# Kernel tuning notes

Hardware: AMD Instinct MI355X
Metric: run time of the kernel (lower is better)

The kernel has to match this reference:

```python
import jax, jax.numpy as jnp
import numpy as np
from jax import lax

B, L, D = 2, 1024, 1024
EXPAND, N, K = 2, 16, 4          # expand, d_state, d_conv
DI = EXPAND * D                  # d_inner = 2048
R = (D + 15) // 16               # dt_rank = 64
EPS = 1e-5


def setup_inputs() -> dict:
    key = jax.random.key(0)
    ks = jax.random.split(key, 8)
    x = jax.random.normal(ks[0], (B, L, D), dtype=jnp.float32)
    ln_w = jnp.ones((D,), jnp.float32)
    ln_b = jnp.zeros((D,), jnp.float32)
    W_in = jax.random.normal(ks[1], (D, 2 * DI), jnp.float32) * (1.0 / np.sqrt(D))
    conv_w = jax.random.normal(ks[2], (DI, K), jnp.float32) * 0.2
    conv_b = jnp.zeros((DI,), jnp.float32)
    W_x = jax.random.normal(ks[3], (DI, R + 2 * N), jnp.float32) * (1.0 / np.sqrt(DI))
    W_dt = jax.random.normal(ks[4], (R, DI), jnp.float32) * (1.0 / np.sqrt(R))
    b_dt = jnp.full((DI,), -4.0, jnp.float32)  # softplus(-4) ~ 0.018 dt init
    A_log = jnp.log(jnp.broadcast_to(jnp.arange(1, N + 1, dtype=jnp.float32), (DI, N)))
    D_param = jnp.ones((DI,), jnp.float32)
    W_out = jax.random.normal(ks[5], (DI, D), jnp.float32) * (1.0 / np.sqrt(DI))
    return {"x": x, "ln_w": ln_w, "ln_b": ln_b, "W_in": W_in, "conv_w": conv_w,
            "conv_b": conv_b, "W_x": W_x, "W_dt": W_dt, "b_dt": b_dt,
            "A_log": A_log, "D_param": D_param, "W_out": W_out}


def _mamba_block(x, ln_w, ln_b, W_in, conv_w, conv_b, W_x, W_dt, b_dt, A_log, D_param, W_out):
    # pre-LayerNorm
    mu = jnp.mean(x, axis=-1, keepdims=True)
    xc = x - mu
    var = jnp.mean(xc * xc, axis=-1, keepdims=True)
    h = xc * lax.rsqrt(var + EPS) * ln_w + ln_b          # [B,L,D]

    xz = h @ W_in                                        # [B,L,2*DI]
    xi, z = xz[..., :DI], xz[..., DI:]

    # depthwise causal conv1d, kernel K, left pad K-1
    xp = jnp.pad(xi, ((0, 0), (K - 1, 0), (0, 0)))
    conv = conv_b
    for k in range(K):
        conv = conv + xp[:, k:k + L, :] * conv_w[:, k]
    u = jax.nn.silu(conv)                                # [B,L,DI]

    proj = u @ W_x                                       # [B,L,R+2N]
    dt_r = proj[..., :R]
    Bm = proj[..., R:R + N]                              # [B,L,N]
    Cm = proj[..., R + N:]                               # [B,L,N]
    dt = jax.nn.softplus(dt_r @ W_dt + b_dt)             # [B,L,DI]

    A = -jnp.exp(A_log)                                  # [DI,N]
    dA = jnp.exp(dt[..., None] * A)                      # [B,L,DI,N]
    dBu = (dt * u)[..., None] * Bm[:, :, None, :]        # [B,L,DI,N]

    def comb(e1, e2):
        a1, b1 = e1
        a2, b2 = e2
        return a1 * a2, a2 * b1 + b2

    _, hs = lax.associative_scan(comb, (dA, dBu), axis=1)  # [B,L,DI,N]
    y = jnp.einsum('bldn,bln->bld', hs, Cm) + u * D_param
    y = y * jax.nn.silu(z)
    return x + y @ W_out


def reference(x, ln_w, ln_b, W_in, conv_w, conv_b, W_x, W_dt, b_dt, A_log, D_param, W_out):
    return _mamba_block(x, ln_w, ln_b, W_in, conv_w, conv_b, W_x, W_dt, b_dt,
                        A_log, D_param, W_out)
```

## Files before the change

### kernel.cpp

```cpp
#include <hip/hip_runtime.h>
#include <hip/hip_bf16.h>
#include <math.h>

#define B_ 2
#define L_ 1024
#define D_ 1024
#define DI_ 2048
#define K_ 4
#define N_ 16
#define R_ 64
#define BL_ (B_ * L_)
#define EPS_ 1e-5f

#define IDX4(l) ((l) + (((l) >> 6) << 2))

typedef __attribute__((ext_vector_type(8))) short short8;
typedef __attribute__((ext_vector_type(4))) float f32x4;

__device__ inline unsigned short f2bf(float f) {
    unsigned u = __float_as_uint(f);
    unsigned r = (u + 0x7fffu + ((u >> 16) & 1u)) >> 16;
    return (unsigned short)r;
}
__device__ inline float bf2f(unsigned short s) {
    return __uint_as_float(((unsigned)s) << 16);
}
__device__ inline float fast_silu(float z) {
    return z * __builtin_amdgcn_rcpf(1.f + __expf(-z));
}
__device__ inline void gl_lds16(const void* g, void* l) {
    __builtin_amdgcn_global_load_lds(
        (const __attribute__((address_space(1))) void*)g,
        (__attribute__((address_space(3))) void*)l, 16, 0, 0);
}

template <int CTRL>
__device__ inline float dpp_shr(float x) {
    return __int_as_float(__builtin_amdgcn_update_dpp(
        0, __float_as_int(x), CTRL, 0xf, 0xf, true));
}
__device__ inline float row16_sum(float p) {
    p += dpp_shr<0x111>(p);
    p += dpp_shr<0x112>(p);
    p += dpp_shr<0x114>(p);
    p += dpp_shr<0x118>(p);
    return p;
}

__global__ void ln_kernel(const float* __restrict__ x, const float* __restrict__ w,
                          const float* __restrict__ b, unsigned short* __restrict__ hb) {
    int row = blockIdx.x;
    const float* xr = x + (size_t)row * D_;
    float4 v = ((const float4*)xr)[threadIdx.x];

    __shared__ float red[4];
    float s = v.x + v.y + v.z + v.w;
    for (int off = 1; off < 64; off <<= 1) s += __shfl_xor(s, off, 64);
    if ((threadIdx.x & 63) == 0) red[threadIdx.x >> 6] = s;
    __syncthreads();
    float mu = (red[0] + red[1] + red[2] + red[3]) * (1.0f / D_);
    __syncthreads();
    float cx = v.x - mu, cy = v.y - mu, cz = v.z - mu, cw = v.w - mu;
    float sq = cx*cx + cy*cy + cz*cz + cw*cw;
    for (int off = 1; off < 64; off <<= 1) sq += __shfl_xor(sq, off, 64);
    if ((threadIdx.x & 63) == 0) red[threadIdx.x >> 6] = sq;
    __syncthreads();
    float var = (red[0] + red[1] + red[2] + red[3]) * (1.0f / D_);
    float rstd = rsqrtf(var + EPS_);

    float4 wv = ((const float4*)w)[threadIdx.x];
    float4 bv = ((const float4*)b)[threadIdx.x];
    ushort4 o;
    o.x = f2bf(cx * rstd * wv.x + bv.x);
    o.y = f2bf(cy * rstd * wv.y + bv.y);
    o.z = f2bf(cz * rstd * wv.z + bv.z);
    o.w = f2bf(cw * rstd * wv.w + bv.w);
    ((ushort4*)(hb + (size_t)row * D_))[threadIdx.x] = o;
}

__global__ void transpose_cast(const float* __restrict__ W, unsigned short* __restrict__ WT,
                               int K, int N) {
    __shared__ float tile[32][33];
    int k0 = blockIdx.y * 32, n0 = blockIdx.x * 32;
    int tr = threadIdx.x >> 5;
    int tc = threadIdx.x & 31;
#pragma unroll
    for (int i = 0; i < 4; ++i)
        tile[tr + i*8][tc] = W[(size_t)(k0 + tr + i*8) * N + n0 + tc];
    __syncthreads();
#pragma unroll
    for (int i = 0; i < 4; ++i)
        WT[(size_t)(n0 + tr + i*8) * K + k0 + tc] = f2bf(tile[tc][tr + i*8]);
}

template <int BN, int MODE>
__global__ __launch_bounds__(256) void mfma_gemm_bt(
        const unsigned short* __restrict__ A,  int lda,
        const unsigned short* __restrict__ BT, int ldb,
        float* __restrict__ C, int ldc, int Kchunk) {
    constexpr int NT = BN / 32;
    __shared__ unsigned short As[128 * 32];
    __shared__ unsigned short Bs[BN * 32];

    int tid = threadIdx.x;
    int wave = tid >> 6, lane = tid & 63;
    int lane15 = lane & 15, quad = lane >> 4;
    int wr = wave >> 1, wc = wave & 1;

    int m0 = blockIdx.y * 128;
    int n0 = blockIdx.x * BN;
    int kbeg = blockIdx.z * Kchunk;
    int kend = kbeg + Kchunk;

    f32x4 acc[4][NT];
#pragma unroll
    for (int i = 0; i < 4; ++i)
#pragma unroll
        for (int j = 0; j < NT; ++j) acc[i][j] = (f32x4){0.f, 0.f, 0.f, 0.f};

    constexpr int ACALLS = 8;
    constexpr int BCALLS = BN * 4 / 64;

    for (int k0 = kbeg; k0 < kend; k0 += 32) {
        __syncthreads();
        for (int c = wave; c < ACALLS + BCALLS; c += 4) {
            if (c < ACALLS) {
                int cell = c * 64 + lane;
                int m = cell >> 2, s = cell & 3;
                int q = s ^ (m & 3) ^ ((m >> 2) & 3);
                gl_lds16(A + (size_t)(m0 + m) * lda + k0 + q * 8, &As[c * 512]);
            } else {
                int cell = (c - ACALLS) * 64 + lane;
                int n = cell >> 2, s = cell & 3;
                int q = s ^ (n & 3) ^ ((n >> 2) & 3);
                gl_lds16(BT + (size_t)(n0 + n) * ldb + k0 + q * 8, &Bs[(c - ACALLS) * 512]);
            }
        }
        __syncthreads();

        short8 af[4], bfr[NT];
#pragma unroll
        for (int i = 0; i < 4; ++i) {
            int m = wr * 64 + i * 16 + lane15;
            int s = quad ^ (m & 3) ^ ((m >> 2) & 3);
            af[i] = *(const short8*)&As[m * 32 + s * 8];
        }
#pragma unroll
        for (int j = 0; j < NT; ++j) {
            int n = wc * (NT * 16) + j * 16 + lane15;
            int s = quad ^ (n & 3) ^ ((n >> 2) & 3);
            bfr[j] = *(const short8*)&Bs[n * 32 + s * 8];
        }
#pragma unroll
        for (int i = 0; i < 4; ++i)
#pragma unroll
            for (int j = 0; j < NT; ++j)
                acc[i][j] = __builtin_amdgcn_mfma_f32_16x16x32_bf16(af[i], bfr[j], acc[i][j], 0, 0, 0);
    }

#pragma unroll
    for (int i = 0; i < 4; ++i) {
        int row = m0 + wr * 64 + i * 16 + quad * 4;
#pragma unroll
        for (int j = 0; j < NT; ++j) {
            int col = n0 + wc * (NT * 16) + j * 16 + lane15;
#pragma unroll
            for (int r = 0; r < 4; ++r) {
                float v = acc[i][j][r];
                size_t off = (size_t)(row + r) * ldc + col;
                if (MODE == 0) C[off] = v;
                else atomicAdd(&C[off], v);
            }
        }
    }
}

template <int EPI>
__global__ __launch_bounds__(256) void gemm_kernel(
        const float* __restrict__ A, int lda,
        const float* __restrict__ Bm, int ldb,
        float* __restrict__ C, int ldc,
        int M, int Nn, int Kk,
        const float* __restrict__ bias) {
    const int BK = 16;
    __shared__ float As[BK][64 + 4];
    __shared__ float Bs[BK][64];

    int tid = threadIdx.x;
    int m0 = blockIdx.y * 64;
    int n0 = blockIdx.x * 64;
    int ar = tid >> 2, ak = (tid & 3) << 2;
    int kb = tid >> 4, bc = (tid & 15) << 2;
    int ty = tid >> 4, tx = tid & 15;

    float acc[4][4] = {};
    for (int k0 = 0; k0 < Kk; k0 += BK) {
        const float* Ap = A + (size_t)(m0 + ar) * lda + (k0 + ak);
        float4 av = *(const float4*)Ap;
        As[ak + 0][ar] = av.x; As[ak + 1][ar] = av.y;
        As[ak + 2][ar] = av.z; As[ak + 3][ar] = av.w;

        const float* Bp = Bm + (size_t)(k0 + kb) * ldb + n0 + bc;
        float4 bv = *(const float4*)Bp;
        Bs[kb][bc + 0] = bv.x; Bs[kb][bc + 1] = bv.y;
        Bs[kb][bc + 2] = bv.z; Bs[kb][bc + 3] = bv.w;
        __syncthreads();
#pragma unroll
        for (int kk = 0; kk < BK; ++kk) {
            float a[4], bb[4];
#pragma unroll
            for (int i = 0; i < 4; ++i) a[i] = As[kk][ty * 4 + i];
#pragma unroll
            for (int j = 0; j < 4; ++j) bb[j] = Bs[kk][tx * 4 + j];
#pragma unroll
            for (int i = 0; i < 4; ++i)
#pragma unroll
                for (int j = 0; j < 4; ++j)
                    acc[i][j] = fmaf(a[i], bb[j], acc[i][j]);
        }
        __syncthreads();
    }
#pragma unroll
    for (int i = 0; i < 4; ++i) {
        int row = m0 + ty * 4 + i;
#pragma unroll
        for (int j = 0; j < 4; ++j) {
            int col = n0 + tx * 4 + j;
            float v = acc[i][j];
            if (EPI == 1) {
                v += bias[col];
                v = fmaxf(v, 0.f) + __logf(1.f + __expf(-fabsf(v)));
            }
            C[(size_t)row * ldc + col] = v;
        }
    }
}

__global__ void conv_silu_kernel(const float* __restrict__ xz, const float* __restrict__ cw,
                                 const float* __restrict__ cb, unsigned short* __restrict__ ub) {
    int idx = blockIdx.x * blockDim.x + threadIdx.x;
    int c = idx & (DI_ - 1);
    int bl = idx >> 11;
    int l = bl & (L_ - 1);
    float4 w4 = ((const float4*)cw)[c];
    float acc = cb[c];
    const float* base = xz + (size_t)bl * (2 * DI_) + c;
    if (l >= 3) {
        acc = fmaf(base[-(size_t)3 * 2 * DI_], w4.x, acc);
        acc = fmaf(base[-(size_t)2 * 2 * DI_], w4.y, acc);
        acc = fmaf(base[-(size_t)1 * 2 * DI_], w4.z, acc);
        acc = fmaf(base[0],                    w4.w, acc);
    } else {
        if (l >= 2) acc = fmaf(*(base - 2 * 2 * DI_), w4.y, acc);
        if (l >= 1) acc = fmaf(*(base - 1 * 2 * DI_), w4.z, acc);
        acc = fmaf(base[0], w4.w, acc);
    }
    ub[idx] = f2bf(fast_silu(acc));
}

__global__ void prep_v3(const float* __restrict__ dt, const unsigned short* __restrict__ ub,
                        const float* __restrict__ xz, const float* __restrict__ Dp,
                        float2* __restrict__ dtduT, unsigned int* __restrict__ szdT) {
    __shared__ float t_dt[32][33];
    __shared__ float t_du[32][33];
    __shared__ unsigned int t_sd[32][33];
    int bl0 = blockIdx.y * 32, c0 = blockIdx.x * 32;
    int r = threadIdx.x >> 5;
    int col = threadIdx.x & 31;
    float dpv = Dp[c0 + col];
#pragma unroll
    for (int i = 0; i < 4; ++i) {
        int bl = bl0 + r + i*8;
        float d = dt[(size_t)bl * DI_ + c0 + col];
        float uu = bf2f(ub[(size_t)bl * DI_ + c0 + col]);
        float z = xz[(size_t)bl * (2 * DI_) + DI_ + c0 + col];
        float sz = fast_silu(z);
        t_dt[r + i*8][col] = d;
        t_du[r + i*8][col] = d * uu;
        t_sd[r + i*8][col] = ((unsigned)f2bf(uu * dpv * sz) << 16) | (unsigned)f2bf(sz);
    }
    __syncthreads();
#pragma unroll
    for (int i = 0; i < 4; ++i) {
        int c = c0 + r + i*8;
        dtduT[(size_t)c * BL_ + bl0 + col] = make_float2(t_dt[col][r + i*8], t_du[col][r + i*8]);
        szdT [(size_t)c * BL_ + bl0 + col] = t_sd[col][r + i*8];
    }
}

__global__ void bct2_kernel(const float* __restrict__ proj, float2* __restrict__ bcti) {
    int t = threadIdx.x;
    int bl = blockIdx.x * 16 + (t >> 4);
    int n = t & 15;
    float Bv = proj[(size_t)bl * 96 + R_ + n];
    float Cv = proj[(size_t)bl * 96 + R_ + N_ + n];
    bcti[(size_t)bl * 16 + n] = make_float2(Bv, Cv);
}

__global__ __launch_bounds__(256) void scan_v4(
        const float2* __restrict__ dtduT, const unsigned int* __restrict__ szdT,
        const float2* __restrict__ bcti, const float* __restrict__ A_log,
        unsigned short* __restrict__ yzT) {
    int bc = blockIdx.x;
    int b = bc >> 11;
    int c = bc & (DI_ - 1);
    int t = threadIdx.x;
    int chunk = t >> 4;
    int n = t & 15;

    __shared__ float dd[(L_ + 32) * 2];
    __shared__ float sA[16][16];
    __shared__ float sB[16][16];
    __shared__ float ps[L_ + 64];

    const size_t tb = (size_t)c * BL_ + (size_t)b * L_;

    {
        int l = t * 4;
        const float4* g = (const float4*)(dtduT + tb + l);
        float4 a0 = g[0], a1 = g[1];
        int il2 = l + ((l >> 6) << 1);
        *(float4*)&dd[il2 * 2]     = a0;
        *(float4*)&dd[il2 * 2 + 4] = a1;
    }
    __syncthreads();

    float A = -__expf(A_log[c * N_ + n]);
    int l0 = chunk * 64;
    const float* ddp = &dd[(l0 + 2 * chunk) * 2];
    const float* bcf = (const float*)(bcti + ((size_t)b * L_ + l0) * 16 + n);

    float a = 1.f, acc = 0.f;
#pragma unroll
    for (int q = 0; q < 16; ++q) {
        float4 d0 = *(const float4*)(ddp + q * 8);
        float4 d1 = *(const float4*)(ddp + q * 8 + 4);
        float b0 = bcf[(q*4 + 0) * 32];
        float b1 = bcf[(q*4 + 1) * 32];
        float b2 = bcf[(q*4 + 2) * 32];
        float b3 = bcf[(q*4 + 3) * 32];
        float e;
        e = __expf(d0.x * A); a *= e; acc = fmaf(e, acc, d0.y * b0);
        e = __expf(d0.z * A); a *= e; acc = fmaf(e, acc, d0.w * b1);
        e = __expf(d1.x * A); a *= e; acc = fmaf(e, acc, d1.y * b2);
        e = __expf(d1.z * A); a *= e; acc = fmaf(e, acc, d1.w * b3);
    }
    sA[chunk][n] = a;
    sB[chunk][n] = acc;
    __syncthreads();

    if (t < 16) {
        float hc = 0.f;
#pragma unroll
        for (int j = 0; j < 16; ++j) {
            float aj = sA[j][t];
            float bj = sB[j][t];
            sB[j][t] = hc;
            hc = fmaf(aj, hc, bj);
        }
    }
    __syncthreads();
    float h = sB[chunk][n];

    float* psb = &ps[IDX4(l0)];
    const float2* bcp = bcti + ((size_t)b * L_ + l0) * 16 + n;
#pragma unroll
    for (int q = 0; q < 16; ++q) {
        float4 d0 = *(const float4*)(ddp + q * 8);
        float4 d1 = *(const float4*)(ddp + q * 8 + 4);
        float2 bc0 = bcp[(q*4 + 0) * 16];
        float2 bc1 = bcp[(q*4 + 1) * 16];
        float2 bc2 = bcp[(q*4 + 2) * 16];
        float2 bc3 = bcp[(q*4 + 3) * 16];
        float e, p0, p1, p2, p3;
        e = __expf(d0.x * A); h = fmaf(e, h, d0.y * bc0.x); p0 = row16_sum(h * bc0.y);
        e = __expf(d0.z * A); h = fmaf(e, h, d0.w * bc1.x); p1 = row16_sum(h * bc1.y);
        e = __expf(d1.x * A); h = fmaf(e, h, d1.y * bc2.x); p2 = row16_sum(h * bc2.y);
        e = __expf(d1.z * A); h = fmaf(e, h, d1.w * bc3.x); p3 = row16_sum(h * bc3.y);
        if (n == 15) *(float4*)&psb[q * 4] = (float4){p0, p1, p2, p3};
    }
    __syncthreads();

    {
        int l = t * 4;
        int il = IDX4(l);
        float4 p4 = *(const float4*)&ps[il];
        uint4 sd4 = *(const uint4*)(szdT + tb + l);
        ushort4 o;
        o.x = f2bf(p4.x * bf2f((unsigned short)(sd4.x & 0xffff)) + bf2f((unsigned short)(sd4.x >> 16)));
        o.y = f2bf(p4.y * bf2f((unsigned short)(sd4.y & 0xffff)) + bf2f((unsigned short)(sd4.y >> 16)));
        o.z = f2bf(p4.z * bf2f((unsigned short)(sd4.z & 0xffff)) + bf2f((unsigned short)(sd4.z >> 16)));
        o.w = f2bf(p4.w * bf2f((unsigned short)(sd4.w & 0xffff)) + bf2f((unsigned short)(sd4.w >> 16)));
        *(ushort4*)(yzT + tb + l) = o;
    }
}

__global__ void transpose_y(const unsigned short* __restrict__ yzT, unsigned short* __restrict__ yz) {
    __shared__ unsigned short t[32][33];
    int c0 = blockIdx.y * 32, bl0 = blockIdx.x * 32;
    int r = threadIdx.x >> 5;
    int col = threadIdx.x & 31;
#pragma unroll
    for (int i = 0; i < 4; ++i)
        t[r + i*8][col] = yzT[(size_t)(c0 + r + i*8) * BL_ + bl0 + col];
    __syncthreads();
#pragma unroll
    for (int i = 0; i < 4; ++i)
        yz[(size_t)(bl0 + r + i*8) * DI_ + c0 + col] = t[col][r + i*8];
}

extern "C" void kernel_launch(void* const* d_in, const int* in_sizes, int n_in,
                              void* d_out, int out_size, void* d_ws, size_t ws_size,
                              hipStream_t stream) {
    const float* x       = (const float*)d_in[0];
    const float* ln_w    = (const float*)d_in[1];
    const float* ln_b    = (const float*)d_in[2];
    const float* W_in    = (const float*)d_in[3];
    const float* conv_w  = (const float*)d_in[4];
    const float* conv_b  = (const float*)d_in[5];
    const float* W_x     = (const float*)d_in[6];
    const float* W_dt    = (const float*)d_in[7];
    const float* b_dt    = (const float*)d_in[8];
    const float* A_log   = (const float*)d_in[9];
    const float* D_param = (const float*)d_in[10];
    const float* W_out   = (const float*)d_in[11];
    float* out = (float*)d_out;

    uint8_t* p = (uint8_t*)d_ws;
    unsigned short* hb    = (unsigned short*)p;  p += (size_t)BL_ * D_ * 2;
    unsigned short* WinT  = (unsigned short*)p;  p += (size_t)4096 * 1024 * 2;
    float*          xz    = (float*)p;           p += (size_t)BL_ * 2 * DI_ * 4;
    unsigned short* ub    = (unsigned short*)p;  p += (size_t)BL_ * DI_ * 2;
    unsigned short* WxT   = (unsigned short*)p;  p += (size_t)96 * DI_ * 2;
    float*          proj  = (float*)p;           p += (size_t)BL_ * 96 * 4;
    float*          dt    = (float*)p;           p += (size_t)BL_ * DI_ * 4;
    unsigned short* WoutT = (unsigned short*)p;  p += (size_t)1024 * DI_ * 2;
    float2*         dtduT = (float2*)p;          p += (size_t)BL_ * DI_ * 8;
    unsigned int*   szdT  = (unsigned int*)p;    p += (size_t)BL_ * DI_ * 4;
    float2*         bcti  = (float2*)p;          p += (size_t)BL_ * 16 * 8;
    unsigned short* yzT   = (unsigned short*)p;  p += (size_t)BL_ * DI_ * 2;
    unsigned short* yzb   = (unsigned short*)d_ws;

    hipMemsetAsync(proj, 0, (size_t)BL_ * 96 * 4, stream);
    hipMemcpyAsync(out, x, (size_t)BL_ * D_ * 4, hipMemcpyDeviceToDevice, stream);

    transpose_cast<<<dim3(4096 / 32, 1024 / 32), 256, 0, stream>>>(W_in, WinT, 1024, 4096);
    transpose_cast<<<dim3(96 / 32, DI_ / 32), 256, 0, stream>>>(W_x, WxT, DI_, 96);
    transpose_cast<<<dim3(1024 / 32, DI_ / 32), 256, 0, stream>>>(W_out, WoutT, DI_, 1024);

    ln_kernel<<<BL_, 256, 0, stream>>>(x, ln_w, ln_b, hb);

    mfma_gemm_bt<128, 0><<<dim3(4096 / 128, BL_ / 128, 1), 256, 0, stream>>>(
        hb, 1024, WinT, 1024, xz, 4096, 1024);

    conv_silu_kernel<<<(BL_ * DI_) / 256, 256, 0, stream>>>(xz, conv_w, conv_b, ub);

    mfma_gemm_bt<96, 1><<<dim3(1, BL_ / 128, 16), 256, 0, stream>>>(
        ub, DI_, WxT, DI_, proj, 96, 128);

    gemm_kernel<1><<<dim3(DI_ / 64, BL_ / 64), 256, 0, stream>>>(
        proj, 96, W_dt, DI_, dt, DI_, BL_, DI_, R_, b_dt);

    prep_v3<<<dim3(DI_ / 32, BL_ / 32), 256, 0, stream>>>(dt, ub, xz, D_param, dtduT, szdT);
    bct2_kernel<<<BL_ / 16, 256, 0, stream>>>(proj, bcti);

    scan_v4<<<B_ * DI_, 256, 0, stream>>>(dtduT, szdT, bcti, A_log, yzT);

    transpose_y<<<dim3(BL_ / 32, DI_ / 32), 256, 0, stream>>>(yzT, yzb);

    mfma_gemm_bt<128, 1><<<dim3(1024 / 128, BL_ / 128, 2), 256, 0, stream>>>(
        yzb, DI_, WoutT, DI_, out, 1024, 1024);
}
```

Measured before the change: 323.6 us.

## Fuse dt GEMM with scan prep, split in-proj epilogue, merge weight casts

The in-projection GEMM epilogue now writes xi in fp32 and silu(z) in bf16 to separate buffers, so later kernels no longer re-read the full fp32 z half. The dt projection GEMM is fused with softplus and the transposed dt/du/skip packing, which removes the fp32 dt round trip and the separate prep kernel. The scan now handles two channels per block and reads B/C straight from proj, so the bct2 kernel goes away. The three weight transposes are merged into one launch. Risks include register and LDS pressure in the fused kernels and strided uncoalesced B/C reads from proj inside the scan.

Result: faster. 286.7 us (-11.4%).

```diff
diff --git a/kernel.cpp b/kernel.cpp
--- a/kernel.cpp
+++ b/kernel.cpp
@@ -78,10 +78,17 @@
     ((ushort4*)(hb + (size_t)row * D_))[threadIdx.x] = o;
 }
 
-__global__ void transpose_cast(const float* __restrict__ W, unsigned short* __restrict__ WT,
-                               int K, int N) {
+__global__ void transpose_cast_all(const float* __restrict__ W_in, const float* __restrict__ W_x,
+                                   const float* __restrict__ W_out,
+                                   unsigned short* __restrict__ WinT, unsigned short* __restrict__ WxT,
+                                   unsigned short* __restrict__ WoutT) {
+    int bid = blockIdx.x;
+    const float* W; unsigned short* WT; int K, N, bx, by;
+    if (bid < 4096)      { W = W_in;  WT = WinT;  K = 1024; N = 4096; bx = bid & 127; by = bid >> 7; }
+    else if (bid < 4288) { int id = bid - 4096; W = W_x;  WT = WxT;  K = DI_; N = 96;   bx = id % 3;  by = id / 3; }
+    else                 { int id = bid - 4288; W = W_out; WT = WoutT; K = DI_; N = 1024; bx = id & 31; by = id >> 5; }
     __shared__ float tile[32][33];
-    int k0 = blockIdx.y * 32, n0 = blockIdx.x * 32;
+    int k0 = by * 32, n0 = bx * 32;
     int tr = threadIdx.x >> 5;
     int tc = threadIdx.x & 31;
 #pragma unroll
@@ -97,7 +104,8 @@
 __global__ __launch_bounds__(256) void mfma_gemm_bt(
         const unsigned short* __restrict__ A,  int lda,
         const unsigned short* __restrict__ BT, int ldb,
-        float* __restrict__ C, int ldc, int Kchunk) {
+        float* __restrict__ C, int ldc, int Kchunk,
+        float* __restrict__ xi, unsigned short* __restrict__ sz) {
     constexpr int NT = BN / 32;
     __shared__ unsigned short As[128 * 32];
     __shared__ unsigned short Bs[BN * 32];
@@ -167,76 +175,21 @@
 #pragma unroll
             for (int r = 0; r < 4; ++r) {
                 float v = acc[i][j][r];
-                size_t off = (size_t)(row + r) * ldc + col;
-                if (MODE == 0) C[off] = v;
-                else atomicAdd(&C[off], v);
+                int rr = row + r;
+                if (MODE == 0) {
+                    C[(size_t)rr * ldc + col] = v;
+                } else if (MODE == 1) {
+                    atomicAdd(&C[(size_t)rr * ldc + col], v);
+                } else {
+                    if (col < DI_) xi[(size_t)rr * DI_ + col] = v;
+                    else           sz[(size_t)rr * DI_ + (col - DI_)] = f2bf(fast_silu(v));
+                }
             }
         }
     }
 }
 
-template <int EPI>
-__global__ __launch_bounds__(256) void gemm_kernel(
-        const float* __restrict__ A, int lda,
-        const float* __restrict__ Bm, int ldb,
-        float* __restrict__ C, int ldc,
-        int M, int Nn, int Kk,
-        const float* __restrict__ bias) {
-    const int BK = 16;
-    __shared__ float As[BK][64 + 4];
-    __shared__ float Bs[BK][64];
-
-    int tid = threadIdx.x;
-    int m0 = blockIdx.y * 64;
-    int n0 = blockIdx.x * 64;
-    int ar = tid >> 2, ak = (tid & 3) << 2;
-    int kb = tid >> 4, bc = (tid & 15) << 2;
-    int ty = tid >> 4, tx = tid & 15;
-
-    float acc[4][4] = {};
-    for (int k0 = 0; k0 < Kk; k0 += BK) {
-        const float* Ap = A + (size_t)(m0 + ar) * lda + (k0 + ak);
-        float4 av = *(const float4*)Ap;
-        As[ak + 0][ar] = av.x; As[ak + 1][ar] = av.y;
-        As[ak + 2][ar] = av.z; As[ak + 3][ar] = av.w;
-
-        const float* Bp = Bm + (size_t)(k0 + kb) * ldb + n0 + bc;
-        float4 bv = *(const float4*)Bp;
-        Bs[kb][bc + 0] = bv.x; Bs[kb][bc + 1] = bv.y;
-        Bs[kb][bc + 2] = bv.z; Bs[kb][bc + 3] = bv.w;
-        __syncthreads();
-#pragma unroll
-        for (int kk = 0; kk < BK; ++kk) {
-            float a[4], bb[4];
-#pragma unroll
-            for (int i = 0; i < 4; ++i) a[i] = As[kk][ty * 4 + i];
-#pragma unroll
-            for (int j = 0; j < 4; ++j) bb[j] = Bs[kk][tx * 4 + j];
-#pragma unroll
-            for (int i = 0; i < 4; ++i)
-#pragma unroll
-                for (int j = 0; j < 4; ++j)
-                    acc[i][j] = fmaf(a[i], bb[j], acc[i][j]);
-        }
-        __syncthreads();
-    }
-#pragma unroll
-    for (int i = 0; i < 4; ++i) {
-        int row = m0 + ty * 4 + i;
-#pragma unroll
-        for (int j = 0; j < 4; ++j) {
-            int col = n0 + tx * 4 + j;
-            float v = acc[i][j];
-            if (EPI == 1) {
-                v += bias[col];
-                v = fmaxf(v, 0.f) + __logf(1.f + __expf(-fabsf(v)));
-            }
-            C[(size_t)row * ldc + col] = v;
-        }
-    }
-}
-
-__global__ void conv_silu_kernel(const float* __restrict__ xz, const float* __restrict__ cw,
+__global__ void conv_silu_kernel(const float* __restrict__ xi, const float* __restrict__ cw,
                                  const float* __restrict__ cb, unsigned short* __restrict__ ub) {
     int idx = blockIdx.x * blockDim.x + threadIdx.x;
     int c = idx & (DI_ - 1);
@@ -244,115 +197,189 @@
     int l = bl & (L_ - 1);
     float4 w4 = ((const float4*)cw)[c];
     float acc = cb[c];
-    const float* base = xz + (size_t)bl * (2 * DI_) + c;
+    const float* base = xi + (size_t)bl * DI_ + c;
     if (l >= 3) {
-        acc = fmaf(base[-(size_t)3 * 2 * DI_], w4.x, acc);
-        acc = fmaf(base[-(size_t)2 * 2 * DI_], w4.y, acc);
-        acc = fmaf(base[-(size_t)1 * 2 * DI_], w4.z, acc);
-        acc = fmaf(base[0],                    w4.w, acc);
+        acc = fmaf(base[-(size_t)3 * DI_], w4.x, acc);
+        acc = fmaf(base[-(size_t)2 * DI_], w4.y, acc);
+        acc = fmaf(base[-(size_t)1 * DI_], w4.z, acc);
+        acc = fmaf(base[0],                w4.w, acc);
     } else {
-        if (l >= 2) acc = fmaf(*(base - 2 * 2 * DI_), w4.y, acc);
-        if (l >= 1) acc = fmaf(*(base - 1 * 2 * DI_), w4.z, acc);
+        if (l >= 2) acc = fmaf(*(base - 2 * DI_), w4.y, acc);
+        if (l >= 1) acc = fmaf(*(base - 1 * DI_), w4.z, acc);
         acc = fmaf(base[0], w4.w, acc);
     }
     ub[idx] = f2bf(fast_silu(acc));
 }
 
-__global__ void prep_v3(const float* __restrict__ dt, const unsigned short* __restrict__ ub,
-                        const float* __restrict__ xz, const float* __restrict__ Dp,
-                        float2* __restrict__ dtduT, unsigned int* __restrict__ szdT) {
-    __shared__ float t_dt[32][33];
-    __shared__ float t_du[32][33];
-    __shared__ unsigned int t_sd[32][33];
-    int bl0 = blockIdx.y * 32, c0 = blockIdx.x * 32;
-    int r = threadIdx.x >> 5;
-    int col = threadIdx.x & 31;
-    float dpv = Dp[c0 + col];
+__global__ __launch_bounds__(256) void dtprep(
+        const float* __restrict__ proj, const float* __restrict__ W_dt,
+        const float* __restrict__ b_dt, const unsigned short* __restrict__ ub,
+        const unsigned short* __restrict__ szb, const float* __restrict__ Dp,
+        float2* __restrict__ dtduT, unsigned int* __restrict__ szdT) {
+    __shared__ alignas(16) unsigned char smem[64 * 65 * 8];
+    float (*As)[68] = reinterpret_cast<float(*)[68]>(smem);
+    float (*Bs)[64] = reinterpret_cast<float(*)[64]>(smem + 4352);
+    float2 (*T2)[65] = reinterpret_cast<float2(*)[65]>(smem);
+    unsigned int (*TU)[65] = reinterpret_cast<unsigned int(*)[65]>(smem);
+
+    int tid = threadIdx.x;
+    int n0 = blockIdx.x * 64;
+    int m0 = blockIdx.y * 64;
+    int ar = tid >> 2, ak = (tid & 3) << 2;
+    int kb = tid >> 4, bc = (tid & 15) << 2;
+    int ty = tid >> 4, tx = tid & 15;
+
+    float acc[4][4] = {};
+#pragma unroll
+    for (int k0 = 0; k0 < R_; k0 += 16) {
+        float4 av = *(const float4*)&proj[(size_t)(m0 + ar) * 96 + k0 + ak];
+        As[ak + 0][ar] = av.x; As[ak + 1][ar] = av.y;
+        As[ak + 2][ar] = av.z; As[ak + 3][ar] = av.w;
+        float4 bv = *(const float4*)&W_dt[(size_t)(k0 + kb) * DI_ + n0 + bc];
+        Bs[kb][bc + 0] = bv.x; Bs[kb][bc + 1] = bv.y;
+        Bs[kb][bc + 2] = bv.z; Bs[kb][bc + 3] = bv.w;
+        __syncthreads();
+#pragma unroll
+        for (int kk = 0; kk < 16; ++kk) {
+            float a[4], bb[4];
+#pragma unroll
+            for (int i = 0; i < 4; ++i) a[i] = As[kk][ty * 4 + i];
+#pragma unroll
+            for (int j = 0; j < 4; ++j) bb[j] = Bs[kk][tx * 4 + j];
+#pragma unroll
+            for (int i = 0; i < 4; ++i)
+#pragma unroll
+                for (int j = 0; j < 4; ++j)
+                    acc[i][j] = fmaf(a[i], bb[j], acc[i][j]);
+        }
+        __syncthreads();
+    }
+
+    float4 bd = *(const float4*)&b_dt[n0 + tx * 4];
+    float4 dp4 = *(const float4*)&Dp[n0 + tx * 4];
+    float bda[4] = {bd.x, bd.y, bd.z, bd.w};
+    float dpa[4] = {dp4.x, dp4.y, dp4.z, dp4.w};
+    float2 d2[4][4];
+    unsigned int su[4][4];
 #pragma unroll
     for (int i = 0; i < 4; ++i) {
-        int bl = bl0 + r + i*8;
-        float d = dt[(size_t)bl * DI_ + c0 + col];
-        float uu = bf2f(ub[(size_t)bl * DI_ + c0 + col]);
-        float z = xz[(size_t)bl * (2 * DI_) + DI_ + c0 + col];
-        float sz = fast_silu(z);
-        t_dt[r + i*8][col] = d;
-        t_du[r + i*8][col] = d * uu;
-        t_sd[r + i*8][col] = ((unsigned)f2bf(uu * dpv * sz) << 16) | (unsigned)f2bf(sz);
-    }
-    __syncthreads();
-#pragma unroll
-    for (int i = 0; i < 4; ++i) {
-        int c = c0 + r + i*8;
-        dtduT[(size_t)c * BL_ + bl0 + col] = make_float2(t_dt[col][r + i*8], t_du[col][r + i*8]);
-        szdT [(size_t)c * BL_ + bl0 + col] = t_sd[col][r + i*8];
-    }
-}
-
-__global__ void bct2_kernel(const float* __restrict__ proj, float2* __restrict__ bcti) {
-    int t = threadIdx.x;
-    int bl = blockIdx.x * 16 + (t >> 4);
-    int n = t & 15;
-    float Bv = proj[(size_t)bl * 96 + R_ + n];
-    float Cv = proj[(size_t)bl * 96 + R_ + N_ + n];
-    bcti[(size_t)bl * 16 + n] = make_float2(Bv, Cv);
-}
-
-__global__ __launch_bounds__(256) void scan_v4(
+        int bl = m0 + ty * 4 + i;
+        ushort4 u4 = *(const ushort4*)&ub[(size_t)bl * DI_ + n0 + tx * 4];
+        ushort4 s4 = *(const ushort4*)&szb[(size_t)bl * DI_ + n0 + tx * 4];
+        unsigned short ua[4] = {u4.x, u4.y, u4.z, u4.w};
+        unsigned short sa[4] = {s4.x, s4.y, s4.z, s4.w};
+#pragma unroll
+        for (int j = 0; j < 4; ++j) {
+            float v = acc[i][j] + bda[j];
+            float dtv = fmaxf(v, 0.f) + __logf(1.f + __expf(-fabsf(v)));
+            float uu = bf2f(ua[j]);
+            float szv = bf2f(sa[j]);
+            d2[i][j] = make_float2(dtv, dtv * uu);
+            su[i][j] = ((unsigned)f2bf(uu * dpa[j] * szv) << 16) | (unsigned)f2bf(szv);
+        }
+    }
+
+#pragma unroll
+    for (int i = 0; i < 4; ++i)
+#pragma unroll
+        for (int j = 0; j < 4; ++j)
+            T2[ty * 4 + i][tx * 4 + j] = d2[i][j];
+    __syncthreads();
+#pragma unroll
+    for (int i = 0; i < 8; ++i) {
+        int c_l = (tid >> 5) + i * 8;
+#pragma unroll
+        for (int jj = 0; jj < 2; ++jj) {
+            int bl_l = (tid & 31) + jj * 32;
+            dtduT[(size_t)(n0 + c_l) * BL_ + m0 + bl_l] = T2[bl_l][c_l];
+        }
+    }
+    __syncthreads();
+
+#pragma unroll
+    for (int i = 0; i < 4; ++i)
+#pragma unroll
+        for (int j = 0; j < 4; ++j)
+            TU[ty * 4 + i][tx * 4 + j] = su[i][j];
+    __syncthreads();
+#pragma unroll
+    for (int i = 0; i < 8; ++i) {
+        int c_l = (tid >> 5) + i * 8;
+#pragma unroll
+        for (int jj = 0; jj < 2; ++jj) {
+            int bl_l = (tid & 31) + jj * 32;
+            szdT[(size_t)(n0 + c_l) * BL_ + m0 + bl_l] = TU[bl_l][c_l];
+        }
+    }
+}
+
+__global__ __launch_bounds__(256) void scan_v5(
         const float2* __restrict__ dtduT, const unsigned int* __restrict__ szdT,
-        const float2* __restrict__ bcti, const float* __restrict__ A_log,
+        const float* __restrict__ proj, const float* __restrict__ A_log,
         unsigned short* __restrict__ yzT) {
     int bc = blockIdx.x;
-    int b = bc >> 11;
-    int c = bc & (DI_ - 1);
+    int b = bc >> 10;
+    int cp = bc & 1023;
     int t = threadIdx.x;
-    int chunk = t >> 4;
     int n = t & 15;
-
-    __shared__ float dd[(L_ + 32) * 2];
-    __shared__ float sA[16][16];
-    __shared__ float sB[16][16];
-    __shared__ float ps[L_ + 64];
-
-    const size_t tb = (size_t)c * BL_ + (size_t)b * L_;
+    int cs = (t >> 4) & 1;
+    int chunk = t >> 5;
+    int c = cp * 2 + cs;
+
+    __shared__ float dd[2][(L_ + 32) * 2];
+    __shared__ float sA[8][32];
+    __shared__ float sB[8][32];
+    __shared__ float ps[2][L_ + 64];
 
     {
-        int l = t * 4;
-        const float4* g = (const float4*)(dtduT + tb + l);
-        float4 a0 = g[0], a1 = g[1];
+        int half = t >> 7;
+        int tt = t & 127;
+        int l = tt * 8;
+        int cload = cp * 2 + half;
+        const float4* g = (const float4*)(dtduT + (size_t)cload * BL_ + (size_t)b * L_ + l);
         int il2 = l + ((l >> 6) << 1);
-        *(float4*)&dd[il2 * 2]     = a0;
-        *(float4*)&dd[il2 * 2 + 4] = a1;
+        float* dst = &dd[half][il2 * 2];
+        *(float4*)(dst + 0)  = g[0];
+        *(float4*)(dst + 4)  = g[1];
+        *(float4*)(dst + 8)  = g[2];
+        *(float4*)(dst + 12) = g[3];
     }
     __syncthreads();
 
     float A = -__expf(A_log[c * N_ + n]);
-    int l0 = chunk * 64;
-    const float* ddp = &dd[(l0 + 2 * chunk) * 2];
-    const float* bcf = (const float*)(bcti + ((size_t)b * L_ + l0) * 16 + n);
+    int l0 = chunk * 128;
+    const float* pB = proj + (size_t)b * L_ * 96 + R_ + n;
+    const float* pC = pB + N_;
 
     float a = 1.f, acc = 0.f;
 #pragma unroll
-    for (int q = 0; q < 16; ++q) {
-        float4 d0 = *(const float4*)(ddp + q * 8);
-        float4 d1 = *(const float4*)(ddp + q * 8 + 4);
-        float b0 = bcf[(q*4 + 0) * 32];
-        float b1 = bcf[(q*4 + 1) * 32];
-        float b2 = bcf[(q*4 + 2) * 32];
-        float b3 = bcf[(q*4 + 3) * 32];
-        float e;
-        e = __expf(d0.x * A); a *= e; acc = fmaf(e, acc, d0.y * b0);
-        e = __expf(d0.z * A); a *= e; acc = fmaf(e, acc, d0.w * b1);
-        e = __expf(d1.x * A); a *= e; acc = fmaf(e, acc, d1.y * b2);
-        e = __expf(d1.z * A); a *= e; acc = fmaf(e, acc, d1.w * b3);
-    }
-    sA[chunk][n] = a;
-    sB[chunk][n] = acc;
-    __syncthreads();
-
-    if (t < 16) {
+    for (int h = 0; h < 2; ++h) {
+        int lb = l0 + h * 64;
+        const float* ddp = &dd[cs][(lb + ((lb >> 6) << 1)) * 2];
+        const float* pBb = pB + (size_t)lb * 96;
+#pragma unroll
+        for (int q = 0; q < 16; ++q) {
+            float4 d0 = *(const float4*)(ddp + q * 8);
+            float4 d1 = *(const float4*)(ddp + q * 8 + 4);
+            float b0 = pBb[(q*4 + 0) * 96];
+            float b1 = pBb[(q*4 + 1) * 96];
+            float b2 = pBb[(q*4 + 2) * 96];
+            float b3 = pBb[(q*4 + 3) * 96];
+            float e;
+            e = __expf(d0.x * A); a *= e; acc = fmaf(e, acc, d0.y * b0);
+            e = __expf(d0.z * A); a *= e; acc = fmaf(e, acc, d0.w * b1);
+            e = __expf(d1.x * A); a *= e; acc = fmaf(e, acc, d1.y * b2);
+            e = __expf(d1.z * A); a *= e; acc = fmaf(e, acc, d1.w * b3);
+        }
+    }
+    sA[chunk][t & 31] = a;
+    sB[chunk][t & 31] = acc;
+    __syncthreads();
+
+    if (t < 32) {
         float hc = 0.f;
 #pragma unroll
-        for (int j = 0; j < 16; ++j) {
+        for (int j = 0; j < 8; ++j) {
             float aj = sA[j][t];
             float bj = sB[j][t];
             sB[j][t] = hc;
@@ -360,38 +387,52 @@
         }
     }
     __syncthreads();
-    float h = sB[chunk][n];
-
-    float* psb = &ps[IDX4(l0)];
-    const float2* bcp = bcti + ((size_t)b * L_ + l0) * 16 + n;
-#pragma unroll
-    for (int q = 0; q < 16; ++q) {
-        float4 d0 = *(const float4*)(ddp + q * 8);
-        float4 d1 = *(const float4*)(ddp + q * 8 + 4);
-        float2 bc0 = bcp[(q*4 + 0) * 16];
-        float2 bc1 = bcp[(q*4 + 1) * 16];
-        float2 bc2 = bcp[(q*4 + 2) * 16];
-        float2 bc3 = bcp[(q*4 + 3) * 16];
-        float e, p0, p1, p2, p3;
-        e = __expf(d0.x * A); h = fmaf(e, h, d0.y * bc0.x); p0 = row16_sum(h * bc0.y);
-        e = __expf(d0.z * A); h = fmaf(e, h, d0.w * bc1.x); p1 = row16_sum(h * bc1.y);
-        e = __expf(d1.x * A); h = fmaf(e, h, d1.y * bc2.x); p2 = row16_sum(h * bc2.y);
-        e = __expf(d1.z * A); h = fmaf(e, h, d1.w * bc3.x); p3 = row16_sum(h * bc3.y);
-        if (n == 15) *(float4*)&psb[q * 4] = (float4){p0, p1, p2, p3};
+    float h = sB[chunk][t & 31];
+
+#pragma unroll
+    for (int hh = 0; hh < 2; ++hh) {
+        int lb = l0 + hh * 64;
+        const float* ddp = &dd[cs][(lb + ((lb >> 6) << 1)) * 2];
+        const float* pBb = pB + (size_t)lb * 96;
+        const float* pCb = pC + (size_t)lb * 96;
+        float* psb = &ps[cs][IDX4(lb)];
+#pragma unroll
+        for (int q = 0; q < 16; ++q) {
+            float4 d0 = *(const float4*)(ddp + q * 8);
+            float4 d1 = *(const float4*)(ddp + q * 8 + 4);
+            float b0 = pBb[(q*4 + 0) * 96], c0 = pCb[(q*4 + 0) * 96];
+            float b1 = pBb[(q*4 + 1) * 96], c1 = pCb[(q*4 + 1) * 96];
+            float b2 = pBb[(q*4 + 2) * 96], c2 = pCb[(q*4 + 2) * 96];
+            float b3 = pBb[(q*4 + 3) * 96], c3 = pCb[(q*4 + 3) * 96];
+            float e, p0, p1, p2, p3;
+            e = __expf(d0.x * A); h = fmaf(e, h, d0.y * b0); p0 = row16_sum(h * c0);
+            e = __expf(d0.z * A); h = fmaf(e, h, d0.w * b1); p1 = row16_sum(h * c1);
+            e = __expf(d1.x * A); h = fmaf(e, h, d1.y * b2); p2 = row16_sum(h * c2);
+            e = __expf(d1.z * A); h = fmaf(e, h, d1.w * b3); p3 = row16_sum(h * c3);
+            if (n == 15) *(float4*)&psb[q * 4] = (float4){p0, p1, p2, p3};
+        }
     }
     __syncthreads();
 
     {
-        int l = t * 4;
-        int il = IDX4(l);
-        float4 p4 = *(const float4*)&ps[il];
-        uint4 sd4 = *(const uint4*)(szdT + tb + l);
-        ushort4 o;
-        o.x = f2bf(p4.x * bf2f((unsigned short)(sd4.x & 0xffff)) + bf2f((unsigned short)(sd4.x >> 16)));
-        o.y = f2bf(p4.y * bf2f((unsigned short)(sd4.y & 0xffff)) + bf2f((unsigned short)(sd4.y >> 16)));
-        o.z = f2bf(p4.z * bf2f((unsigned short)(sd4.z & 0xffff)) + bf2f((unsigned short)(sd4.z >> 16)));
-        o.w = f2bf(p4.w * bf2f((unsigned short)(sd4.w & 0xffff)) + bf2f((unsigned short)(sd4.w >> 16)));
-        *(ushort4*)(yzT + tb + l) = o;
+        int half = t >> 7;
+        int tt = t & 127;
+        int l = tt * 8;
+        int c_out = cp * 2 + half;
+        size_t tb = (size_t)c_out * BL_ + (size_t)b * L_;
+        const float* pp = &ps[half][IDX4(l)];
+        ushort4 o[2];
+#pragma unroll
+        for (int g = 0; g < 2; ++g) {
+            float4 p4 = *(const float4*)(pp + g * 4);
+            uint4 sd4 = *(const uint4*)(szdT + tb + l + g * 4);
+            o[g].x = f2bf(p4.x * bf2f((unsigned short)(sd4.x & 0xffff)) + bf2f((unsigned short)(sd4.x >> 16)));
+            o[g].y = f2bf(p4.y * bf2f((unsigned short)(sd4.y & 0xffff)) + bf2f((unsigned short)(sd4.y >> 16)));
+            o[g].z = f2bf(p4.z * bf2f((unsigned short)(sd4.z & 0xffff)) + bf2f((unsigned short)(sd4.z >> 16)));
+            o[g].w = f2bf(p4.w * bf2f((unsigned short)(sd4.w & 0xffff)) + bf2f((unsigned short)(sd4.w >> 16)));
+        }
+        *(ushort4*)(yzT + tb + l) = o[0];
+        *(ushort4*)(yzT + tb + l + 4) = o[1];
     }
 }
 
@@ -429,45 +470,39 @@
     uint8_t* p = (uint8_t*)d_ws;
     unsigned short* hb    = (unsigned short*)p;  p += (size_t)BL_ * D_ * 2;
     unsigned short* WinT  = (unsigned short*)p;  p += (size_t)4096 * 1024 * 2;
-    float*          xz    = (float*)p;           p += (size_t)BL_ * 2 * DI_ * 4;
+    float*          xib   = (float*)p;           p += (size_t)BL_ * DI_ * 4;
+    unsigned short* szb   = (unsigned short*)p;  p += (size_t)BL_ * DI_ * 2;
     unsigned short* ub    = (unsigned short*)p;  p += (size_t)BL_ * DI_ * 2;
     unsigned short* WxT   = (unsigned short*)p;  p += (size_t)96 * DI_ * 2;
     float*          proj  = (float*)p;           p += (size_t)BL_ * 96 * 4;
-    float*          dt    = (float*)p;           p += (size_t)BL_ * DI_ * 4;
     unsigned short* WoutT = (unsigned short*)p;  p += (size_t)1024 * DI_ * 2;
     float2*         dtduT = (float2*)p;          p += (size_t)BL_ * DI_ * 8;
     unsigned int*   szdT  = (unsigned int*)p;    p += (size_t)BL_ * DI_ * 4;
-    float2*         bcti  = (float2*)p;          p += (size_t)BL_ * 16 * 8;
     unsigned short* yzT   = (unsigned short*)p;  p += (size_t)BL_ * DI_ * 2;
     unsigned short* yzb   = (unsigned short*)d_ws;
 
     hipMemsetAsync(proj, 0, (size_t)BL_ * 96 * 4, stream);
     hipMemcpyAsync(out, x, (size_t)BL_ * D_ * 4, hipMemcpyDeviceToDevice, stream);
 
-    transpose_cast<<<dim3(4096 / 32, 1024 / 32), 256, 0, stream>>>(W_in, WinT, 1024, 4096);
-    transpose_cast<<<dim3(96 / 32, DI_ / 32), 256, 0, stream>>>(W_x, WxT, DI_, 96);
-    transpose_cast<<<dim3(1024 / 32, DI_ / 32), 256, 0, stream>>>(W_out, WoutT, DI_, 1024);
+    transpose_cast_all<<<6336, 256, 0, stream>>>(W_in, W_x, W_out, WinT, WxT, WoutT);
 
     ln_kernel<<<BL_, 256, 0, stream>>>(x, ln_w, ln_b, hb);
 
-    mfma_gemm_bt<128, 0><<<dim3(4096 / 128, BL_ / 128, 1), 256, 0, stream>>>(
-        hb, 1024, WinT, 1024, xz, 4096, 1024);
-
-    conv_silu_kernel<<<(BL_ * DI_) / 256, 256, 0, stream>>>(xz, conv_w, conv_b, ub);
+    mfma_gemm_bt<128, 3><<<dim3(4096 / 128, BL_ / 128, 1), 256, 0, stream>>>(
+        hb, 1024, WinT, 1024, nullptr, 0, 1024, xib, szb);
+
+    conv_silu_kernel<<<(BL_ * DI_) / 256, 256, 0, stream>>>(xib, conv_w, conv_b, ub);
 
     mfma_gemm_bt<96, 1><<<dim3(1, BL_ / 128, 16), 256, 0, stream>>>(
-        ub, DI_, WxT, DI_, proj, 96, 128);
-
-    gemm_kernel<1><<<dim3(DI_ / 64, BL_ / 64), 256, 0, stream>>>(
-        proj, 96, W_dt, DI_, dt, DI_, BL_, DI_, R_, b_dt);
-
-    prep_v3<<<dim3(DI_ / 32, BL_ / 32), 256, 0, stream>>>(dt, ub, xz, D_param, dtduT, szdT);
-    bct2_kernel<<<BL_ / 16, 256, 0, stream>>>(proj, bcti);
-
-    scan_v4<<<B_ * DI_, 256, 0, stream>>>(dtduT, szdT, bcti, A_log, yzT);
+        ub, DI_, WxT, DI_, proj, 96, 128, nullptr, nullptr);
+
+    dtprep<<<dim3(DI_ / 64, BL_ / 64), 256, 0, stream>>>(
+        proj, W_dt, b_dt, ub, szb, D_param, dtduT, szdT);
+
+    scan_v5<<<B_ * DI_ / 2, 256, 0, stream>>>(dtduT, szdT, proj, A_log, yzT);
 
     transpose_y<<<dim3(BL_ / 32, DI_ / 32), 256, 0, stream>>>(yzT, yzb);
 
     mfma_gemm_bt<128, 1><<<dim3(1024 / 128, BL_ / 128, 2), 256, 0, stream>>>(
-        yzb, DI_, WoutT, DI_, out, 1024, 1024);
-}
+        yzb, DI_, WoutT, DI_, out, 1024, 1024, nullptr, nullptr);
+}
```
